# Kernel optimization log

Hardware: AMD Instinct MI355X
Metric: run time of the kernel (lower is better)

Reference implementation:

```python
import jax, jax.numpy as jnp
import numpy as np

# LIF / memristor constants (from AnalogNeuron and ResistiveMemoryElement defaults)
T, B, N, M = 1024, 16, 2048, 512
DT = 1e-7            # simulation timestep (s)
CMEM = 1e-12         # membrane capacitance (F)
G_LEAK = 1e-9        # leak conductance (S)
VTH = 0.7            # threshold voltage (V)
VRESET = 0.0         # reset voltage
REFRAC = 1e-6        # refractory period (s) -> 10 steps
TAU_ADAPT = 1e-4     # adaptation time constant (s)
ADAPT_INC = 5e-11    # adaptation current increment on spike (A)
GAIN = 1.0           # gain_mismatch
OFFSET = 0.0         # offset_voltage
I_NOISE_STD = 1e-12  # current_noise std (A)
V_NOISE_STD = 1e-3   # voltage_noise std (V)
READ_V = 0.1         # memristor read voltage (V)
MAX_R = 1e8          # max resistance -> min conductance clip
COND_NOISE_STD = 0.1118  # sqrt(0.1^2 + 0.05^2): device variation + read noise, relative
EXT_SCALE = 1e-6     # external drive scale (A): dV/step ~ 0.1 V


def setup_inputs() -> dict:
    key = jax.random.key(0)
    k1, k2, k3, k4, k5 = jax.random.split(key, 5)
    ext_current = jax.random.normal(k1, (T, B, N), dtype=jnp.float32) * EXT_SCALE
    i_noise = jax.random.normal(k2, (T, B, N), dtype=jnp.float32) * I_NOISE_STD
    v_noise = jax.random.normal(k3, (T, B, N), dtype=jnp.float32) * V_NOISE_STD
    # conductances of a 2048x512 RRAM crossbar: resistances 1e5..1e7 ohm -> G in [1e-7, 1e-5] S
    G = jax.random.uniform(k4, (N, M), dtype=jnp.float32, minval=1e-7, maxval=1e-5)
    cond_noise = jax.random.normal(k5, (N, M), dtype=jnp.float32)
    return {"ext_current": ext_current, "i_noise": i_noise, "v_noise": v_noise,
            "G": G, "cond_noise": cond_noise}


def reference(ext_current, i_noise, v_noise, G, cond_noise):
    dtype = ext_current.dtype
    t_steps = ext_current.shape[0]
    t_arr = jnp.arange(t_steps, dtype=dtype) * DT  # wall-clock time per step

    def step(carry, xs):
        V, A, last_spike = carry          # [B,N] each
        ext, inz, vnz, t = xs
        active = (t - last_spike) >= REFRAC
        total_I = ext - A + inz           # excitatory - adaptation + noise current
        Vn = V + DT * (total_I - G_LEAK * V) / CMEM + vnz + OFFSET
        An = A * (1.0 - DT / TAU_ADAPT)   # A += dt*(-A/tau)
        V1 = jnp.where(active, Vn, V)
        A1 = jnp.where(active, An, A)
        spike = active & (V1 >= VTH * GAIN)
        V2 = jnp.where(spike, VRESET, V1)
        A2 = jnp.where(spike, A1 + ADAPT_INC, A1)
        ls2 = jnp.where(spike, t, last_spike)
        return (V2, A2, ls2), spike.astype(dtype)

    V0 = jnp.zeros(ext_current.shape[1:], dtype)
    A0 = jnp.zeros_like(V0)
    ls0 = jnp.full_like(V0, -1e9)  # last_spike_time = -inf
    (Vf, Af, _), spikes = jax.lax.scan(step, (V0, A0, ls0),
                                       (ext_current, i_noise, v_noise, t_arr))
    rates = spikes.mean(axis=0)  # [B,N] firing rates
    # memristive crossbar read: noisy conductance, clipped at 1/max_R, read at READ_V
    Gn = jnp.maximum(1.0 / MAX_R, G * (1.0 + COND_NOISE_STD * cond_noise))
    readout = rates @ (Gn * READ_V)  # [B,M]
    return readout
```

## Files before the change

kernel.cpp:

```cpp
#include <hip/hip_runtime.h>

namespace {

constexpr int T_STEPS = 1024;
constexpr int BATCH   = 16;
constexpr int NNEUR   = 2048;
constexpr int MCOLS   = 512;
constexpr int BN      = BATCH * NNEUR;

constexpr double DT_D   = 1e-7;
constexpr double CMEM_D = 1e-12;
constexpr double GLK_D  = 1e-9;
constexpr double TAU_D  = 1e-4;

constexpr float DT_F     = (float)DT_D;
constexpr float CMEM_F   = (float)CMEM_D;
constexpr float GLEAK_F  = (float)GLK_D;
constexpr float VTH_F    = (float)(0.7 * 1.0);
constexpr float REFRAC_F = (float)1e-6;
constexpr float AINC_F   = (float)5e-11;
constexpr float DECAY_F  = (float)(1.0 - DT_D / TAU_D);
constexpr float VRESET_F = 0.0f;

constexpr int C_STEPS = 16;
constexpr int NBUF    = T_STEPS / C_STEPS;
constexpr int RING    = 5;
constexpr int AHEAD   = 4;
constexpr int LPB     = 12;

}

#define LIF_STEP(ec, ic, vc, tidx)                                         \
    do {                                                                   \
        float t      = (float)(tidx) * DT_F;                               \
        bool  active = (t - ls) >= REFRAC_F;                               \
        float totI   = ((ec) - A) + (ic);                                  \
        float Vn     = (V + (DT_F * (totI - GLEAK_F * V)) / CMEM_F) + (vc);\
        float An     = A * DECAY_F;                                        \
        float V1     = active ? Vn : V;                                    \
        float A1     = active ? An : A;                                    \
        bool  spike  = active && (V1 >= VTH_F);                            \
        V  = spike ? VRESET_F : V1;                                        \
        A  = spike ? (A1 + AINC_F) : A1;                                   \
        ls = spike ? t : ls;                                               \
        count += spike ? 1 : 0;                                            \
    } while (0)

__global__ __launch_bounds__(64) void lif_sim_kernel(
    const float* __restrict__ ext,
    const float* __restrict__ inz,
    const float* __restrict__ vnz,
    float* __restrict__ rates)
{
    __shared__ float lds[RING][3][C_STEPS][64];

    const int lane = threadIdx.x;
    const int g0   = blockIdx.x * 64;

    const int tsub = lane >> 4;
    const int nsub = (lane & 15) * 4;

    auto issue = [&](int j) {
        const int slot = j % RING;
#pragma unroll
        for (int a = 0; a < 3; ++a) {
            const float* base = (a == 0) ? ext : ((a == 1) ? inz : vnz);
#pragma unroll
            for (int q = 0; q < 4; ++q) {
                const float* gp = base +
                    (size_t)(j * C_STEPS + q * 4 + tsub) * BN + (g0 + nsub);
                __builtin_amdgcn_global_load_lds(
                    (const __attribute__((address_space(1))) void*)gp,
                    (__attribute__((address_space(3))) void*)&lds[slot][a][q * 4][0],
                    16, 0, 0);
            }
        }
    };

    float V = 0.0f, A = 0.0f, ls = -1e9f;
    int count = 0;

    for (int j = 0; j < AHEAD; ++j) issue(j);

    for (int k = 0; k < NBUF; ++k) {
        if (k + AHEAD < NBUF) issue(k + AHEAD);

        const int rem = NBUF - 1 - k;
        const int nb  = (rem < AHEAD) ? rem : AHEAD;
        switch (nb) {
            case 4: asm volatile("s_waitcnt vmcnt(48)" ::: "memory"); break;
            case 3: asm volatile("s_waitcnt vmcnt(36)" ::: "memory"); break;
            case 2: asm volatile("s_waitcnt vmcnt(24)" ::: "memory"); break;
            case 1: asm volatile("s_waitcnt vmcnt(12)" ::: "memory"); break;
            default: asm volatile("s_waitcnt vmcnt(0)" ::: "memory"); break;
        }
        __builtin_amdgcn_sched_barrier(0);

        const int slot = k % RING;
#pragma unroll
        for (int c = 0; c < C_STEPS; ++c) {
            float ec = lds[slot][0][c][lane];
            float ic = lds[slot][1][c][lane];
            float vc = lds[slot][2][c][lane];
            LIF_STEP(ec, ic, vc, k * C_STEPS + c);
        }
    }

    rates[g0 + lane] = (float)count * (1.0f / 1024.0f);
}

constexpr int KC   = 8;
constexpr int KCH  = NNEUR / KC;
constexpr int KSUB = 4;
constexpr int KPT  = KCH / KSUB;

__global__ __launch_bounds__(256) void readout_partial_kernel(
    const float* __restrict__ rates,
    const float* __restrict__ G,
    const float* __restrict__ cn,
    float* __restrict__ part)
{
    __shared__ float red[KSUB][64][BATCH + 1];

    const int tid = threadIdx.x;
    const int ml  = tid & 63;
    const int s   = tid >> 6;
    const int m   = blockIdx.x * 64 + ml;
    const int kc  = blockIdx.y;
    const int k0  = kc * KCH + s * KPT;

    float acc[BATCH];
#pragma unroll
    for (int b = 0; b < BATCH; ++b) acc[b] = 0.0f;

#pragma unroll 4
    for (int k = k0; k < k0 + KPT; ++k) {
        float g = G[(size_t)k * MCOLS + m];
        float c = cn[(size_t)k * MCOLS + m];
        float w = fmaxf(1e-8f, g * (1.0f + 0.1118f * c)) * 0.1f;
#pragma unroll
        for (int b = 0; b < BATCH; ++b) {
            acc[b] = fmaf(rates[b * NNEUR + k], w, acc[b]);
        }
    }

#pragma unroll
    for (int b = 0; b < BATCH; ++b) red[s][ml][b] = acc[b];
    __syncthreads();

    if (s == 0) {
#pragma unroll
        for (int b = 0; b < BATCH; ++b) {
            float v = ((red[0][ml][b] + red[1][ml][b]) + red[2][ml][b]) + red[3][ml][b];
            part[((size_t)kc * BATCH + b) * MCOLS + m] = v;
        }
    }
}

__global__ __launch_bounds__(256) void readout_reduce_kernel(
    const float* __restrict__ part,
    float* __restrict__ out)
{
    const int i = blockIdx.x * 256 + threadIdx.x;
    float s = 0.0f;
#pragma unroll
    for (int kc = 0; kc < KC; ++kc) {
        s += part[kc * (BATCH * MCOLS) + i];
    }
    out[i] = s;
}

extern "C" void kernel_launch(void* const* d_in, const int* in_sizes, int n_in,
                              void* d_out, int out_size, void* d_ws, size_t ws_size,
                              hipStream_t stream)
{
    const float* ext = (const float*)d_in[0];
    const float* inz = (const float*)d_in[1];
    const float* vnz = (const float*)d_in[2];
    const float* G   = (const float*)d_in[3];
    const float* cn  = (const float*)d_in[4];
    float* out = (float*)d_out;

    float* rates = (float*)d_ws;
    float* part  = rates + BN;

    lif_sim_kernel<<<BN / 64, 64, 0, stream>>>(ext, inz, vnz, rates);
    readout_partial_kernel<<<dim3(MCOLS / 64, KC), 256, 0, stream>>>(rates, G, cn, part);
    readout_reduce_kernel<<<(BATCH * MCOLS) / 256, 256, 0, stream>>>(part, out);
}
```

Baseline: 126.3 us.

## Share LIF input staging across four waves with cooperative LDS loads

The LIF kernel moves from 64-thread blocks to 256-thread blocks covering 256 neurons. All four waves now jointly fill a shared LDS ring, and each load instruction reads one contiguous 1 KB row segment. A workgroup barrier is added per chunk, and the prefetch is issued after that barrier, with the chunk size and ring depth retuned. This aims for wider coalesced global reads, but it quarters the block count, which may leave CUs idle on a bandwidth-bound kernel, and it adds a barrier every 8 steps.

```diff
diff --git a/kernel.cpp b/kernel.cpp
--- a/kernel.cpp
+++ b/kernel.cpp
@@ -9,24 +9,23 @@
 constexpr int BN      = BATCH * NNEUR;
 
 constexpr double DT_D   = 1e-7;
-constexpr double CMEM_D = 1e-12;
-constexpr double GLK_D  = 1e-9;
 constexpr double TAU_D  = 1e-4;
 
-constexpr float DT_F     = (float)DT_D;
-constexpr float CMEM_F   = (float)CMEM_D;
-constexpr float GLEAK_F  = (float)GLK_D;
-constexpr float VTH_F    = (float)(0.7 * 1.0);
-constexpr float REFRAC_F = (float)1e-6;
-constexpr float AINC_F   = (float)5e-11;
+constexpr float DT_F     = 1e-7f;
+constexpr float CMEM_F   = 1e-12f;
+constexpr float GLEAK_F  = 1e-9f;
+constexpr float VTH_F    = 0.7f;
+constexpr float REFRAC_F = 1e-6f;
+constexpr float AINC_F   = 5e-11f;
 constexpr float DECAY_F  = (float)(1.0 - DT_D / TAU_D);
 constexpr float VRESET_F = 0.0f;
 
-constexpr int C_STEPS = 16;
+constexpr int NPB     = 256;
+constexpr int C_STEPS = 8;
 constexpr int NBUF    = T_STEPS / C_STEPS;
-constexpr int RING    = 5;
-constexpr int AHEAD   = 4;
-constexpr int LPB     = 12;
+constexpr int RING    = 6;
+constexpr int AHEAD   = 5;
+constexpr int LPB_W   = 6;
 
 }
 
@@ -46,34 +45,32 @@
         count += spike ? 1 : 0;                                            \
     } while (0)
 
-__global__ __launch_bounds__(64) void lif_sim_kernel(
+__global__ __launch_bounds__(256) void lif_sim_kernel(
     const float* __restrict__ ext,
     const float* __restrict__ inz,
     const float* __restrict__ vnz,
     float* __restrict__ rates)
 {
-    __shared__ float lds[RING][3][C_STEPS][64];
+    __shared__ float smem[RING][3][C_STEPS][NPB];
 
-    const int lane = threadIdx.x;
-    const int g0   = blockIdx.x * 64;
-
-    const int tsub = lane >> 4;
-    const int nsub = (lane & 15) * 4;
+    const int tid  = threadIdx.x;
+    const int lane = tid & 63;
+    const int w    = tid >> 6;
+    const int n0   = blockIdx.x * NPB;
 
     auto issue = [&](int j) {
         const int slot = j % RING;
 #pragma unroll
-        for (int a = 0; a < 3; ++a) {
+        for (int l = 0; l < LPB_W; ++l) {
+            const int li = w * LPB_W + l;
+            const int a  = li % 3;
+            const int tt = li / 3;
             const float* base = (a == 0) ? ext : ((a == 1) ? inz : vnz);
-#pragma unroll
-            for (int q = 0; q < 4; ++q) {
-                const float* gp = base +
-                    (size_t)(j * C_STEPS + q * 4 + tsub) * BN + (g0 + nsub);
-                __builtin_amdgcn_global_load_lds(
-                    (const __attribute__((address_space(1))) void*)gp,
-                    (__attribute__((address_space(3))) void*)&lds[slot][a][q * 4][0],
-                    16, 0, 0);
-            }
+            const float* gp = base + (size_t)(j * C_STEPS + tt) * BN + (n0 + lane * 4);
+            __builtin_amdgcn_global_load_lds(
+                (const __attribute__((address_space(1))) void*)gp,
+                (__attribute__((address_space(3))) void*)&smem[slot][a][tt][0],
+                16, 0, 0);
         }
     };
 
@@ -83,30 +80,31 @@
     for (int j = 0; j < AHEAD; ++j) issue(j);
 
     for (int k = 0; k < NBUF; ++k) {
-        if (k + AHEAD < NBUF) issue(k + AHEAD);
-
         const int rem = NBUF - 1 - k;
-        const int nb  = (rem < AHEAD) ? rem : AHEAD;
+        const int nb  = (rem < AHEAD - 1) ? rem : (AHEAD - 1);
         switch (nb) {
-            case 4: asm volatile("s_waitcnt vmcnt(48)" ::: "memory"); break;
-            case 3: asm volatile("s_waitcnt vmcnt(36)" ::: "memory"); break;
-            case 2: asm volatile("s_waitcnt vmcnt(24)" ::: "memory"); break;
-            case 1: asm volatile("s_waitcnt vmcnt(12)" ::: "memory"); break;
+            case 4: asm volatile("s_waitcnt vmcnt(24)" ::: "memory"); break;
+            case 3: asm volatile("s_waitcnt vmcnt(18)" ::: "memory"); break;
+            case 2: asm volatile("s_waitcnt vmcnt(12)" ::: "memory"); break;
+            case 1: asm volatile("s_waitcnt vmcnt(6)"  ::: "memory"); break;
             default: asm volatile("s_waitcnt vmcnt(0)" ::: "memory"); break;
         }
+        __builtin_amdgcn_s_barrier();
         __builtin_amdgcn_sched_barrier(0);
+
+        if (k + AHEAD < NBUF) issue(k + AHEAD);
 
         const int slot = k % RING;
 #pragma unroll
         for (int c = 0; c < C_STEPS; ++c) {
-            float ec = lds[slot][0][c][lane];
-            float ic = lds[slot][1][c][lane];
-            float vc = lds[slot][2][c][lane];
+            float ec = smem[slot][0][c][w * 64 + lane];
+            float ic = smem[slot][1][c][w * 64 + lane];
+            float vc = smem[slot][2][c][w * 64 + lane];
             LIF_STEP(ec, ic, vc, k * C_STEPS + c);
         }
     }
 
-    rates[g0 + lane] = (float)count * (1.0f / 1024.0f);
+    rates[n0 + tid] = (float)count * (1.0f / 1024.0f);
 }
 
 constexpr int KC   = 8;
@@ -184,7 +182,7 @@
     float* rates = (float*)d_ws;
     float* part  = rates + BN;
 
-    lif_sim_kernel<<<BN / 64, 64, 0, stream>>>(ext, inz, vnz, rates);
+    lif_sim_kernel<<<BN / NPB, 256, 0, stream>>>(ext, inz, vnz, rates);
     readout_partial_kernel<<<dim3(MCOLS / 64, KC), 256, 0, stream>>>(rates, G, cn, part);
     readout_reduce_kernel<<<(BATCH * MCOLS) / 256, 256, 0, stream>>>(part, out);
 }
```

After: 170.8 us. +35.2%, slower.
